# Optimization experiments

Hardware: AMD Instinct MI355X
Metric: run time of the kernel (lower is better)

## Reference

```python
import jax, jax.numpy as jnp
import numpy as np

N_CODES = 512
D = 8
BETA = 0.25


def setup_inputs() -> dict:
    key = jax.random.key(0)
    k1, k2 = jax.random.split(key)
    z = jax.random.normal(k1, (8, D, 16, 64, 64), dtype=jnp.float32)
    # torch init: uniform(-1/n_codes, 1/n_codes)
    codebook = jax.random.uniform(
        k2, (N_CODES, D), dtype=jnp.float32,
        minval=-1.0 / N_CODES, maxval=1.0 / N_CODES)
    return {"z": z, "codebook": codebook}


def reference(z, codebook):
    B, Dc, T, H, W = z.shape
    # [B, T, H, W, D] -> [N, D]
    z_flat = jnp.transpose(z, (0, 2, 3, 4, 1)).reshape(-1, Dc)
    z2 = jnp.sum(z_flat * z_flat, axis=1, keepdims=True)          # [N, 1]
    e2 = jnp.sum(codebook * codebook, axis=1)[None, :]            # [1, K]
    ze = z_flat @ codebook.T                                      # [N, K]
    dists = z2 + e2 - 2.0 * ze
    idx = jnp.argmin(dists, axis=1)                               # [N]
    z_q = jnp.transpose(codebook[idx].reshape(B, T, H, W, Dc), (0, 4, 1, 2, 3))
    commit = jnp.mean((jax.lax.stop_gradient(z_q) - z) ** 2)
    codebk = jnp.mean((z_q - jax.lax.stop_gradient(z)) ** 2)
    vq_loss = codebk + BETA * commit
    z_q_st = z + jax.lax.stop_gradient(z_q - z)
    return z_q_st, vq_loss, idx.reshape(B, T, H, W)
```

## Files before the change

kernel.cpp:

```cpp
#include <hip/hip_runtime.h>


#define NPTS      524288
#define KCODES    512
#define DDIM      8
#define CH_STRIDE 65536
#define B_STRIDE  524288
#define BLK       512
#define NWAVES    8
#define NTILES    32
#define CMAX      4
#define NLOSS     64
#define FLT_BIG   3.402823466e+38f

typedef short bf8 __attribute__((ext_vector_type(8)));
typedef float f4  __attribute__((ext_vector_type(4)));

__device__ __forceinline__ unsigned short f2bf(float f) {
    unsigned u = __float_as_uint(f);
    unsigned r = u + 0x7fffu + ((u >> 16) & 1u);
    return (unsigned short)(r >> 16);
}
__device__ __forceinline__ float bf2f(unsigned short h) {
    return __uint_as_float(((unsigned)h) << 16);
}

__device__ __forceinline__ float np_sumsq8(const float* x) {
    float p0 = __fmul_rn(x[0], x[0]);
    float p1 = __fmul_rn(x[1], x[1]);
    float p2 = __fmul_rn(x[2], x[2]);
    float p3 = __fmul_rn(x[3], x[3]);
    float p4 = __fmul_rn(x[4], x[4]);
    float p5 = __fmul_rn(x[5], x[5]);
    float p6 = __fmul_rn(x[6], x[6]);
    float p7 = __fmul_rn(x[7], x[7]);
    return __fadd_rn(__fadd_rn(__fadd_rn(p0, p1), __fadd_rn(p2, p3)),
                     __fadd_rn(__fadd_rn(p4, p5), __fadd_rn(p6, p7)));
}

__device__ __forceinline__ float np_dist(const float* __restrict__ cb,
                                         const float* __restrict__ e2f,
                                         int k, const float* zv, float z2) {
    const float* c = cb + (size_t)k * DDIM;
    float ze = 0.0f;
    #pragma unroll
    for (int j = 0; j < DDIM; ++j) ze = __fmaf_rn(zv[j], c[j], ze);
    return __fmaf_rn(-2.0f, ze, __fadd_rn(z2, e2f[k]));
}

__global__ void prep(const float* __restrict__ cb, float* __restrict__ e2f,
                     unsigned short* __restrict__ wsB,
                     float* __restrict__ loss_ws) {
    const int tid = blockIdx.x * 256 + threadIdx.x;
    if (tid < NLOSS) loss_ws[tid] = 0.0f;
    const int t    = tid >> 6;
    const int lane = tid & 63;
    const int quad = lane >> 4;
    const int colc = lane & 15;
    const int n    = t * 16 + colc;
    float row[DDIM];
    #pragma unroll
    for (int j = 0; j < DDIM; ++j) row[j] = cb[n * DDIM + j];
    const float e2 = np_sumsq8(row);
    if (quad == 3) e2f[n] = e2;

    unsigned short sh[8];
    #pragma unroll
    for (int j = 0; j < 8; ++j) {
        const unsigned short eh = f2bf(row[j]);
        const unsigned short el = f2bf(__fsub_rn(row[j], bf2f(eh)));
        sh[j] = (quad == 1) ? el : eh;
    }
    if (quad == 3) {
        const unsigned short e2h = f2bf(e2);
        const unsigned short e2l = f2bf(__fsub_rn(e2, bf2f(e2h)));
        sh[0] = e2h; sh[1] = e2l;
        #pragma unroll
        for (int j = 2; j < 8; ++j) sh[j] = 0;
    }
    unsigned short* dst = wsB + (size_t)(t * 64 + lane) * 8;
    #pragma unroll
    for (int j = 0; j < 8; ++j) dst[j] = sh[j];
}

__global__ __launch_bounds__(BLK, 4) void vq_main(
    const float* __restrict__ z, const float* __restrict__ cb,
    const float* __restrict__ e2f, const unsigned short* __restrict__ wsB,
    float* __restrict__ out_zq, float* __restrict__ loss_ws,
    float* __restrict__ out_idx)
{
    __shared__ int            ccnt[BLK];
    __shared__ unsigned short clist[BLK][CMAX];
    __shared__ float          wsum[NWAVES];

    const int tid  = threadIdx.x;
    const int wave = tid >> 6;
    const int lane = tid & 63;
    const int quad = lane >> 4;
    const int col  = lane & 15;

    ccnt[tid] = 0;

    const int n = blockIdx.x * BLK + tid;
    const int b = n >> 16;
    const int s = n & 65535;
    const float* zp = z + (size_t)b * B_STRIDE + s;
    float zv[DDIM];
    #pragma unroll
    for (int j = 0; j < DDIM; ++j) zv[j] = zp[(size_t)j * CH_STRIDE];
    const float z2 = np_sumsq8(zv);

    float zmax = z2;
    #pragma unroll
    for (int mk = 1; mk <= 32; mk <<= 1) zmax = fmaxf(zmax, __shfl_xor(zmax, mk, 64));
    const float eps = zmax * 6e-7f + 3e-6f;

    unsigned pkz[8];
    #pragma unroll
    for (int j = 0; j < 8; ++j) {
        const unsigned short hh = f2bf(zv[j]);
        const float zh = bf2f(hh);
        const float zl = __fsub_rn(zv[j], zh);
        const unsigned short ah = f2bf(-2.0f * zh);
        const unsigned short al = f2bf(-2.0f * zl);
        pkz[j] = (unsigned)ah | ((unsigned)al << 16);
    }

    bf8 af0, af1, af2, af3;
#define MK_AFRAG(AF, Q)                                                        \
    {                                                                          \
        const int srcl = (Q)*16 + col;                                         \
        _Pragma("unroll")                                                      \
        for (int j = 0; j < 8; ++j) {                                          \
            const unsigned w = (unsigned)__shfl((int)pkz[j], srcl, 64);        \
            const unsigned us = (quad == 2) ? (w >> 16) : (w & 0xFFFFu);       \
            AF[j] = (short)us;                                                 \
        }                                                                      \
        if (quad == 3) AF = (bf8){(short)0x3F80, (short)0x3F80, 0, 0, 0, 0, 0, 0}; \
    }
    MK_AFRAG(af0, 0) MK_AFRAG(af1, 1) MK_AFRAG(af2, 2) MK_AFRAG(af3, 3)

    const bf8* __restrict__ Bp = (const bf8*)wsB;

    f4 mn0 = (f4){FLT_BIG, FLT_BIG, FLT_BIG, FLT_BIG};
    f4 mn1 = mn0, mn2 = mn0, mn3 = mn0;
    #pragma unroll 4
    for (int t = 0; t < NTILES; ++t) {
        const bf8 bfrag = Bp[t * 64 + lane];
        f4 zero = (f4){0.0f, 0.0f, 0.0f, 0.0f};
        const f4 a0 = __builtin_amdgcn_mfma_f32_16x16x32_bf16(af0, bfrag, zero, 0, 0, 0);
        const f4 a1 = __builtin_amdgcn_mfma_f32_16x16x32_bf16(af1, bfrag, zero, 0, 0, 0);
        const f4 a2 = __builtin_amdgcn_mfma_f32_16x16x32_bf16(af2, bfrag, zero, 0, 0, 0);
        const f4 a3 = __builtin_amdgcn_mfma_f32_16x16x32_bf16(af3, bfrag, zero, 0, 0, 0);
        #pragma unroll
        for (int r = 0; r < 4; ++r) {
            mn0[r] = fminf(mn0[r], a0[r]); mn1[r] = fminf(mn1[r], a1[r]);
            mn2[r] = fminf(mn2[r], a2[r]); mn3[r] = fminf(mn3[r], a3[r]);
        }
    }
    #pragma unroll
    for (int mk = 1; mk <= 8; mk <<= 1) {
        #pragma unroll
        for (int r = 0; r < 4; ++r) {
            mn0[r] = fminf(mn0[r], __shfl_xor(mn0[r], mk, 64));
            mn1[r] = fminf(mn1[r], __shfl_xor(mn1[r], mk, 64));
            mn2[r] = fminf(mn2[r], __shfl_xor(mn2[r], mk, 64));
            mn3[r] = fminf(mn3[r], __shfl_xor(mn3[r], mk, 64));
        }
    }
    #pragma unroll
    for (int r = 0; r < 4; ++r) {
        mn0[r] += eps; mn1[r] += eps; mn2[r] += eps; mn3[r] += eps;
    }

    const int pbase = wave * 64 + quad * 4;
    #pragma unroll 4
    for (int t = 0; t < NTILES; ++t) {
        const bf8 bfrag = Bp[t * 64 + lane];
        f4 zero = (f4){0.0f, 0.0f, 0.0f, 0.0f};
        const f4 a0 = __builtin_amdgcn_mfma_f32_16x16x32_bf16(af0, bfrag, zero, 0, 0, 0);
        const f4 a1 = __builtin_amdgcn_mfma_f32_16x16x32_bf16(af1, bfrag, zero, 0, 0, 0);
        const f4 a2 = __builtin_amdgcn_mfma_f32_16x16x32_bf16(af2, bfrag, zero, 0, 0, 0);
        const f4 a3 = __builtin_amdgcn_mfma_f32_16x16x32_bf16(af3, bfrag, zero, 0, 0, 0);
        const unsigned short code = (unsigned short)(t * 16 + col);
#define PUSH(AQ, MQ, Q)                                                        \
    {                                                                          \
        const bool c0 = AQ[0] <= MQ[0], c1 = AQ[1] <= MQ[1];                   \
        const bool c2 = AQ[2] <= MQ[2], c3 = AQ[3] <= MQ[3];                   \
        if (c0 | c1 | c2 | c3) {                                               \
            const int pt = pbase + (Q)*16;                                     \
            if (c0) { int p = atomicAdd(&ccnt[pt + 0], 1); if (p < CMAX) clist[pt + 0][p] = code; } \
            if (c1) { int p = atomicAdd(&ccnt[pt + 1], 1); if (p < CMAX) clist[pt + 1][p] = code; } \
            if (c2) { int p = atomicAdd(&ccnt[pt + 2], 1); if (p < CMAX) clist[pt + 2][p] = code; } \
            if (c3) { int p = atomicAdd(&ccnt[pt + 3], 1); if (p < CMAX) clist[pt + 3][p] = code; } \
        }                                                                      \
    }
        PUSH(a0, mn0, 0) PUSH(a1, mn1, 1) PUSH(a2, mn2, 2) PUSH(a3, mn3, 3)
    }

    asm volatile("s_waitcnt lgkmcnt(0)" ::: "memory");

    const int cnt = ccnt[tid];
    int bidx;
    if (cnt == 1) {
        bidx = clist[tid][0];
    } else if (cnt <= CMAX) {
        float best = FLT_BIG; bidx = 0;
        for (int i = 0; i < cnt; ++i) {
            const int k = clist[tid][i];
            const float d = np_dist(cb, e2f, k, zv, z2);
            if (d < best || (d == best && k < bidx)) { best = d; bidx = k; }
        }
    } else {
        float best = FLT_BIG; bidx = 0;
        for (int k = 0; k < KCODES; ++k) {
            const float d = np_dist(cb, e2f, k, zv, z2);
            if (d < best) { best = d; bidx = k; }
        }
    }
    out_idx[n] = (float)bidx;

    const float* cw = cb + (size_t)bidx * DDIM;
    float* op = out_zq + (size_t)b * B_STRIDE + s;
    float lsum = 0.0f;
    #pragma unroll
    for (int j = 0; j < DDIM; ++j) {
        const float zq = cw[j];
        const float t  = __fsub_rn(zq, zv[j]);
        op[(size_t)j * CH_STRIDE] = __fadd_rn(zv[j], t);
        lsum = __fmaf_rn(t, t, lsum);
    }

    #pragma unroll
    for (int off = 32; off > 0; off >>= 1) lsum += __shfl_down(lsum, off, 64);
    if (lane == 0) wsum[wave] = lsum;
    __syncthreads();
    if (tid == 0) {
        float bs = 0.0f;
        #pragma unroll
        for (int w = 0; w < NWAVES; ++w) bs += wsum[w];
        atomicAdd(&loss_ws[blockIdx.x & (NLOSS - 1)], bs);
    }
}

__global__ void loss_fin(const float* __restrict__ loss_ws,
                         float* __restrict__ out_loss) {
    const int lane = threadIdx.x;
    float v = loss_ws[lane];
    #pragma unroll
    for (int off = 32; off > 0; off >>= 1) v += __shfl_down(v, off, 64);
    if (lane == 0) *out_loss = v * (1.25f / 4194304.0f);
}

extern "C" void kernel_launch(void* const* d_in, const int* in_sizes, int n_in,
                              void* d_out, int out_size, void* d_ws, size_t ws_size,
                              hipStream_t stream) {
    const float* z  = (const float*)d_in[0];
    const float* cb = (const float*)d_in[1];
    float* out      = (float*)d_out;
    float* out_zq   = out;
    float* out_loss = out + 4194304;
    float* out_idx  = out + 4194305;
    float* e2f            = (float*)d_ws;
    unsigned short* wsB   = (unsigned short*)((char*)d_ws + 2048);
    float* loss_ws        = (float*)((char*)d_ws + 2048 + 32768);

    prep<<<8, 256, 0, stream>>>(cb, e2f, wsB, loss_ws);
    vq_main<<<NPTS / BLK, BLK, 0, stream>>>(z, cb, e2f, wsB,
                                            out_zq, loss_ws, out_idx);
    loss_fin<<<1, 64, 0, stream>>>(loss_ws, out_loss);
}
```

Baseline: 123.7 us.

## Process two point sets per thread to reuse codebook fragments across MFMAs

Halves the block size to 256 threads while keeping 512 points per block, so each thread handles two points. Every codebook B-fragment loaded from global memory now feeds eight MFMAs instead of four, cutting fragment loads and loop overhead per point. The cost is roughly double the live registers (two sets of A fragments and running minima), which may lower occupancy. The launch bound changes to 256 threads with a minimum of 2 blocks.

```diff
diff --git a/kernel.cpp b/kernel.cpp
--- a/kernel.cpp
+++ b/kernel.cpp
@@ -6,8 +6,9 @@
 #define DDIM      8
 #define CH_STRIDE 65536
 #define B_STRIDE  524288
-#define BLK       512
-#define NWAVES    8
+#define BLK       256
+#define NWAVES    4
+#define PPB       512
 #define NTILES    32
 #define CMAX      4
 #define NLOSS     64
@@ -83,14 +84,14 @@
     for (int j = 0; j < 8; ++j) dst[j] = sh[j];
 }
 
-__global__ __launch_bounds__(BLK, 4) void vq_main(
+__global__ __launch_bounds__(BLK, 2) void vq_main(
     const float* __restrict__ z, const float* __restrict__ cb,
     const float* __restrict__ e2f, const unsigned short* __restrict__ wsB,
     float* __restrict__ out_zq, float* __restrict__ loss_ws,
     float* __restrict__ out_idx)
 {
-    __shared__ int            ccnt[BLK];
-    __shared__ unsigned short clist[BLK][CMAX];
+    __shared__ int            ccnt[PPB];
+    __shared__ unsigned short clist[PPB][CMAX];
     __shared__ float          wsum[NWAVES];
 
     const int tid  = threadIdx.x;
@@ -99,136 +100,197 @@
     const int quad = lane >> 4;
     const int col  = lane & 15;
 
-    ccnt[tid] = 0;
-
-    const int n = blockIdx.x * BLK + tid;
-    const int b = n >> 16;
-    const int s = n & 65535;
-    const float* zp = z + (size_t)b * B_STRIDE + s;
-    float zv[DDIM];
-    #pragma unroll
-    for (int j = 0; j < DDIM; ++j) zv[j] = zp[(size_t)j * CH_STRIDE];
-    const float z2 = np_sumsq8(zv);
-
-    float zmax = z2;
+    ccnt[tid]       = 0;
+    ccnt[tid + BLK] = 0;
+
+    const int base = blockIdx.x * PPB;
+    const int n0 = base + tid;
+    const int n1 = n0 + BLK;
+    const int b0 = n0 >> 16, s0 = n0 & 65535;
+    const int b1 = n1 >> 16, s1 = n1 & 65535;
+    const float* zp0 = z + (size_t)b0 * B_STRIDE + s0;
+    const float* zp1 = z + (size_t)b1 * B_STRIDE + s1;
+    float zva[DDIM], zvb[DDIM];
+    #pragma unroll
+    for (int j = 0; j < DDIM; ++j) {
+        zva[j] = zp0[(size_t)j * CH_STRIDE];
+        zvb[j] = zp1[(size_t)j * CH_STRIDE];
+    }
+    const float z2a = np_sumsq8(zva);
+    const float z2b = np_sumsq8(zvb);
+
+    float zmax = fmaxf(z2a, z2b);
     #pragma unroll
     for (int mk = 1; mk <= 32; mk <<= 1) zmax = fmaxf(zmax, __shfl_xor(zmax, mk, 64));
     const float eps = zmax * 6e-7f + 3e-6f;
 
-    unsigned pkz[8];
+    unsigned pka[8], pkb[8];
     #pragma unroll
     for (int j = 0; j < 8; ++j) {
-        const unsigned short hh = f2bf(zv[j]);
-        const float zh = bf2f(hh);
-        const float zl = __fsub_rn(zv[j], zh);
-        const unsigned short ah = f2bf(-2.0f * zh);
-        const unsigned short al = f2bf(-2.0f * zl);
-        pkz[j] = (unsigned)ah | ((unsigned)al << 16);
-    }
-
-    bf8 af0, af1, af2, af3;
-#define MK_AFRAG(AF, Q)                                                        \
+        {
+            const unsigned short hh = f2bf(zva[j]);
+            const float zh = bf2f(hh);
+            const float zl = __fsub_rn(zva[j], zh);
+            const unsigned short ah = f2bf(-2.0f * zh);
+            const unsigned short al = f2bf(-2.0f * zl);
+            pka[j] = (unsigned)ah | ((unsigned)al << 16);
+        }
+        {
+            const unsigned short hh = f2bf(zvb[j]);
+            const float zh = bf2f(hh);
+            const float zl = __fsub_rn(zvb[j], zh);
+            const unsigned short ah = f2bf(-2.0f * zh);
+            const unsigned short al = f2bf(-2.0f * zl);
+            pkb[j] = (unsigned)ah | ((unsigned)al << 16);
+        }
+    }
+
+    bf8 af0a, af1a, af2a, af3a, af0b, af1b, af2b, af3b;
+#define MK_AFRAG(AF, Q, PK)                                                    \
     {                                                                          \
         const int srcl = (Q)*16 + col;                                         \
         _Pragma("unroll")                                                      \
         for (int j = 0; j < 8; ++j) {                                          \
-            const unsigned w = (unsigned)__shfl((int)pkz[j], srcl, 64);        \
+            const unsigned w = (unsigned)__shfl((int)PK[j], srcl, 64);         \
             const unsigned us = (quad == 2) ? (w >> 16) : (w & 0xFFFFu);       \
             AF[j] = (short)us;                                                 \
         }                                                                      \
         if (quad == 3) AF = (bf8){(short)0x3F80, (short)0x3F80, 0, 0, 0, 0, 0, 0}; \
     }
-    MK_AFRAG(af0, 0) MK_AFRAG(af1, 1) MK_AFRAG(af2, 2) MK_AFRAG(af3, 3)
+    MK_AFRAG(af0a, 0, pka) MK_AFRAG(af1a, 1, pka)
+    MK_AFRAG(af2a, 2, pka) MK_AFRAG(af3a, 3, pka)
+    MK_AFRAG(af0b, 0, pkb) MK_AFRAG(af1b, 1, pkb)
+    MK_AFRAG(af2b, 2, pkb) MK_AFRAG(af3b, 3, pkb)
 
     const bf8* __restrict__ Bp = (const bf8*)wsB;
 
-    f4 mn0 = (f4){FLT_BIG, FLT_BIG, FLT_BIG, FLT_BIG};
-    f4 mn1 = mn0, mn2 = mn0, mn3 = mn0;
-    #pragma unroll 4
+    f4 mA0 = (f4){FLT_BIG, FLT_BIG, FLT_BIG, FLT_BIG};
+    f4 mA1 = mA0, mA2 = mA0, mA3 = mA0;
+    f4 mB0 = mA0, mB1 = mA0, mB2 = mA0, mB3 = mA0;
+    #pragma unroll 2
     for (int t = 0; t < NTILES; ++t) {
         const bf8 bfrag = Bp[t * 64 + lane];
         f4 zero = (f4){0.0f, 0.0f, 0.0f, 0.0f};
-        const f4 a0 = __builtin_amdgcn_mfma_f32_16x16x32_bf16(af0, bfrag, zero, 0, 0, 0);
-        const f4 a1 = __builtin_amdgcn_mfma_f32_16x16x32_bf16(af1, bfrag, zero, 0, 0, 0);
-        const f4 a2 = __builtin_amdgcn_mfma_f32_16x16x32_bf16(af2, bfrag, zero, 0, 0, 0);
-        const f4 a3 = __builtin_amdgcn_mfma_f32_16x16x32_bf16(af3, bfrag, zero, 0, 0, 0);
+        const f4 dA0 = __builtin_amdgcn_mfma_f32_16x16x32_bf16(af0a, bfrag, zero, 0, 0, 0);
+        const f4 dA1 = __builtin_amdgcn_mfma_f32_16x16x32_bf16(af1a, bfrag, zero, 0, 0, 0);
+        const f4 dA2 = __builtin_amdgcn_mfma_f32_16x16x32_bf16(af2a, bfrag, zero, 0, 0, 0);
+        const f4 dA3 = __builtin_amdgcn_mfma_f32_16x16x32_bf16(af3a, bfrag, zero, 0, 0, 0);
+        const f4 dB0 = __builtin_amdgcn_mfma_f32_16x16x32_bf16(af0b, bfrag, zero, 0, 0, 0);
+        const f4 dB1 = __builtin_amdgcn_mfma_f32_16x16x32_bf16(af1b, bfrag, zero, 0, 0, 0);
+        const f4 dB2 = __builtin_amdgcn_mfma_f32_16x16x32_bf16(af2b, bfrag, zero, 0, 0, 0);
+        const f4 dB3 = __builtin_amdgcn_mfma_f32_16x16x32_bf16(af3b, bfrag, zero, 0, 0, 0);
         #pragma unroll
         for (int r = 0; r < 4; ++r) {
-            mn0[r] = fminf(mn0[r], a0[r]); mn1[r] = fminf(mn1[r], a1[r]);
-            mn2[r] = fminf(mn2[r], a2[r]); mn3[r] = fminf(mn3[r], a3[r]);
+            mA0[r] = fminf(mA0[r], dA0[r]); mA1[r] = fminf(mA1[r], dA1[r]);
+            mA2[r] = fminf(mA2[r], dA2[r]); mA3[r] = fminf(mA3[r], dA3[r]);
+            mB0[r] = fminf(mB0[r], dB0[r]); mB1[r] = fminf(mB1[r], dB1[r]);
+            mB2[r] = fminf(mB2[r], dB2[r]); mB3[r] = fminf(mB3[r], dB3[r]);
         }
     }
     #pragma unroll
     for (int mk = 1; mk <= 8; mk <<= 1) {
         #pragma unroll
         for (int r = 0; r < 4; ++r) {
-            mn0[r] = fminf(mn0[r], __shfl_xor(mn0[r], mk, 64));
-            mn1[r] = fminf(mn1[r], __shfl_xor(mn1[r], mk, 64));
-            mn2[r] = fminf(mn2[r], __shfl_xor(mn2[r], mk, 64));
-            mn3[r] = fminf(mn3[r], __shfl_xor(mn3[r], mk, 64));
+            mA0[r] = fminf(mA0[r], __shfl_xor(mA0[r], mk, 64));
+            mA1[r] = fminf(mA1[r], __shfl_xor(mA1[r], mk, 64));
+            mA2[r] = fminf(mA2[r], __shfl_xor(mA2[r], mk, 64));
+            mA3[r] = fminf(mA3[r], __shfl_xor(mA3[r], mk, 64));
+            mB0[r] = fminf(mB0[r], __shfl_xor(mB0[r], mk, 64));
+            mB1[r] = fminf(mB1[r], __shfl_xor(mB1[r], mk, 64));
+            mB2[r] = fminf(mB2[r], __shfl_xor(mB2[r], mk, 64));
+            mB3[r] = fminf(mB3[r], __shfl_xor(mB3[r], mk, 64));
         }
     }
     #pragma unroll
     for (int r = 0; r < 4; ++r) {
-        mn0[r] += eps; mn1[r] += eps; mn2[r] += eps; mn3[r] += eps;
-    }
-
-    const int pbase = wave * 64 + quad * 4;
-    #pragma unroll 4
+        mA0[r] += eps; mA1[r] += eps; mA2[r] += eps; mA3[r] += eps;
+        mB0[r] += eps; mB1[r] += eps; mB2[r] += eps; mB3[r] += eps;
+    }
+
+    const int pb0 = wave * 64 + quad * 4;
+    const int pb1 = BLK + pb0;
+    #pragma unroll 2
     for (int t = 0; t < NTILES; ++t) {
         const bf8 bfrag = Bp[t * 64 + lane];
         f4 zero = (f4){0.0f, 0.0f, 0.0f, 0.0f};
-        const f4 a0 = __builtin_amdgcn_mfma_f32_16x16x32_bf16(af0, bfrag, zero, 0, 0, 0);
-        const f4 a1 = __builtin_amdgcn_mfma_f32_16x16x32_bf16(af1, bfrag, zero, 0, 0, 0);
-        const f4 a2 = __builtin_amdgcn_mfma_f32_16x16x32_bf16(af2, bfrag, zero, 0, 0, 0);
-        const f4 a3 = __builtin_amdgcn_mfma_f32_16x16x32_bf16(af3, bfrag, zero, 0, 0, 0);
+        const f4 dA0 = __builtin_amdgcn_mfma_f32_16x16x32_bf16(af0a, bfrag, zero, 0, 0, 0);
+        const f4 dA1 = __builtin_amdgcn_mfma_f32_16x16x32_bf16(af1a, bfrag, zero, 0, 0, 0);
+        const f4 dA2 = __builtin_amdgcn_mfma_f32_16x16x32_bf16(af2a, bfrag, zero, 0, 0, 0);
+        const f4 dA3 = __builtin_amdgcn_mfma_f32_16x16x32_bf16(af3a, bfrag, zero, 0, 0, 0);
+        const f4 dB0 = __builtin_amdgcn_mfma_f32_16x16x32_bf16(af0b, bfrag, zero, 0, 0, 0);
+        const f4 dB1 = __builtin_amdgcn_mfma_f32_16x16x32_bf16(af1b, bfrag, zero, 0, 0, 0);
+        const f4 dB2 = __builtin_amdgcn_mfma_f32_16x16x32_bf16(af2b, bfrag, zero, 0, 0, 0);
+        const f4 dB3 = __builtin_amdgcn_mfma_f32_16x16x32_bf16(af3b, bfrag, zero, 0, 0, 0);
         const unsigned short code = (unsigned short)(t * 16 + col);
-#define PUSH(AQ, MQ, Q)                                                        \
+#define PUSH(AQ, MQ, Q, PB)                                                    \
     {                                                                          \
         const bool c0 = AQ[0] <= MQ[0], c1 = AQ[1] <= MQ[1];                   \
         const bool c2 = AQ[2] <= MQ[2], c3 = AQ[3] <= MQ[3];                   \
         if (c0 | c1 | c2 | c3) {                                               \
-            const int pt = pbase + (Q)*16;                                     \
+            const int pt = (PB) + (Q)*16;                                      \
             if (c0) { int p = atomicAdd(&ccnt[pt + 0], 1); if (p < CMAX) clist[pt + 0][p] = code; } \
             if (c1) { int p = atomicAdd(&ccnt[pt + 1], 1); if (p < CMAX) clist[pt + 1][p] = code; } \
             if (c2) { int p = atomicAdd(&ccnt[pt + 2], 1); if (p < CMAX) clist[pt + 2][p] = code; } \
             if (c3) { int p = atomicAdd(&ccnt[pt + 3], 1); if (p < CMAX) clist[pt + 3][p] = code; } \
         }                                                                      \
     }
-        PUSH(a0, mn0, 0) PUSH(a1, mn1, 1) PUSH(a2, mn2, 2) PUSH(a3, mn3, 3)
+        PUSH(dA0, mA0, 0, pb0) PUSH(dA1, mA1, 1, pb0)
+        PUSH(dA2, mA2, 2, pb0) PUSH(dA3, mA3, 3, pb0)
+        PUSH(dB0, mB0, 0, pb1) PUSH(dB1, mB1, 1, pb1)
+        PUSH(dB2, mB2, 2, pb1) PUSH(dB3, mB3, 3, pb1)
     }
 
     asm volatile("s_waitcnt lgkmcnt(0)" ::: "memory");
 
-    const int cnt = ccnt[tid];
-    int bidx;
-    if (cnt == 1) {
-        bidx = clist[tid][0];
-    } else if (cnt <= CMAX) {
-        float best = FLT_BIG; bidx = 0;
-        for (int i = 0; i < cnt; ++i) {
-            const int k = clist[tid][i];
-            const float d = np_dist(cb, e2f, k, zv, z2);
-            if (d < best || (d == best && k < bidx)) { best = d; bidx = k; }
-        }
-    } else {
-        float best = FLT_BIG; bidx = 0;
-        for (int k = 0; k < KCODES; ++k) {
-            const float d = np_dist(cb, e2f, k, zv, z2);
-            if (d < best) { best = d; bidx = k; }
-        }
-    }
-    out_idx[n] = (float)bidx;
-
-    const float* cw = cb + (size_t)bidx * DDIM;
-    float* op = out_zq + (size_t)b * B_STRIDE + s;
+    auto resolve = [&](int slot, const float* zv, float z2) -> int {
+        const int cnt = ccnt[slot];
+        int bidx;
+        if (cnt == 1) {
+            bidx = clist[slot][0];
+        } else if (cnt <= CMAX) {
+            float best = FLT_BIG; bidx = 0;
+            for (int i = 0; i < cnt; ++i) {
+                const int k = clist[slot][i];
+                const float d = np_dist(cb, e2f, k, zv, z2);
+                if (d < best || (d == best && k < bidx)) { best = d; bidx = k; }
+            }
+        } else {
+            float best = FLT_BIG; bidx = 0;
+            for (int k = 0; k < KCODES; ++k) {
+                const float d = np_dist(cb, e2f, k, zv, z2);
+                if (d < best) { best = d; bidx = k; }
+            }
+        }
+        return bidx;
+    };
+
+    const int bidx0 = resolve(tid, zva, z2a);
+    const int bidx1 = resolve(tid + BLK, zvb, z2b);
+    out_idx[n0] = (float)bidx0;
+    out_idx[n1] = (float)bidx1;
+
     float lsum = 0.0f;
-    #pragma unroll
-    for (int j = 0; j < DDIM; ++j) {
-        const float zq = cw[j];
-        const float t  = __fsub_rn(zq, zv[j]);
-        op[(size_t)j * CH_STRIDE] = __fadd_rn(zv[j], t);
-        lsum = __fmaf_rn(t, t, lsum);
+    {
+        const float* cw = cb + (size_t)bidx0 * DDIM;
+        float* op = out_zq + (size_t)b0 * B_STRIDE + s0;
+        #pragma unroll
+        for (int j = 0; j < DDIM; ++j) {
+            const float zq = cw[j];
+            const float t  = __fsub_rn(zq, zva[j]);
+            op[(size_t)j * CH_STRIDE] = __fadd_rn(zva[j], t);
+            lsum = __fmaf_rn(t, t, lsum);
+        }
+    }
+    {
+        const float* cw = cb + (size_t)bidx1 * DDIM;
+        float* op = out_zq + (size_t)b1 * B_STRIDE + s1;
+        #pragma unroll
+        for (int j = 0; j < DDIM; ++j) {
+            const float zq = cw[j];
+            const float t  = __fsub_rn(zq, zvb[j]);
+            op[(size_t)j * CH_STRIDE] = __fadd_rn(zvb[j], t);
+            lsum = __fmaf_rn(t, t, lsum);
+        }
     }
 
     #pragma unroll
@@ -266,7 +328,7 @@
     float* loss_ws        = (float*)((char*)d_ws + 2048 + 32768);
 
     prep<<<8, 256, 0, stream>>>(cb, e2f, wsB, loss_ws);
-    vq_main<<<NPTS / BLK, BLK, 0, stream>>>(z, cb, e2f, wsB,
+    vq_main<<<NPTS / PPB, BLK, 0, stream>>>(z, cb, e2f, wsB,
                                             out_zq, loss_ws, out_idx);
     loss_fin<<<1, 64, 0, stream>>>(loss_ws, out_loss);
 }
```

Measured after the change: 148.1 us. +19.7%, slower.

## Stage codebook B-fragments in LDS and double-buffer two tiles per iteration

Applied to the files above, without the earlier changes.

Copies the pre-packed bf16 codebook fragments (32 KB) from global memory into shared memory once per block, then reads B fragments from LDS instead of global/L2. Both MFMA passes now process two tiles per iteration with register prefetch of the next pair and a combined min-check before candidate pushes. CMAX is raised to 8 so fewer points fall back to the full 512-code scan. The extra 32 KB of LDS per block plus the larger candidate list may reduce occupancy below the launch-bounds target of 4 blocks.

```diff
diff --git a/kernel.cpp b/kernel.cpp
--- a/kernel.cpp
+++ b/kernel.cpp
@@ -9,7 +9,7 @@
 #define BLK       512
 #define NWAVES    8
 #define NTILES    32
-#define CMAX      4
+#define CMAX      8
 #define NLOSS     64
 #define FLT_BIG   3.402823466e+38f
 
@@ -89,6 +89,7 @@
     float* __restrict__ out_zq, float* __restrict__ loss_ws,
     float* __restrict__ out_idx)
 {
+    __shared__ unsigned short ldsB[NTILES * 64 * 8];
     __shared__ int            ccnt[BLK];
     __shared__ unsigned short clist[BLK][CMAX];
     __shared__ float          wsum[NWAVES];
@@ -99,8 +100,6 @@
     const int quad = lane >> 4;
     const int col  = lane & 15;
 
-    ccnt[tid] = 0;
-
     const int n = blockIdx.x * BLK + tid;
     const int b = n >> 16;
     const int s = n & 65535;
@@ -108,6 +107,16 @@
     float zv[DDIM];
     #pragma unroll
     for (int j = 0; j < DDIM; ++j) zv[j] = zp[(size_t)j * CH_STRIDE];
+
+    {
+        const uint4* src = (const uint4*)wsB;
+        uint4* dst = (uint4*)ldsB;
+        #pragma unroll
+        for (int q = 0; q < 4; ++q)
+            dst[tid + q * BLK] = src[tid + q * BLK];
+    }
+    ccnt[tid] = 0;
+
     const float z2 = np_sumsq8(zv);
 
     float zmax = z2;
@@ -140,22 +149,30 @@
     }
     MK_AFRAG(af0, 0) MK_AFRAG(af1, 1) MK_AFRAG(af2, 2) MK_AFRAG(af3, 3)
 
-    const bf8* __restrict__ Bp = (const bf8*)wsB;
+    __syncthreads();
+
+    const bf8* __restrict__ Bp = (const bf8*)ldsB;
+    const f4 zero = (f4){0.0f, 0.0f, 0.0f, 0.0f};
 
     f4 mn0 = (f4){FLT_BIG, FLT_BIG, FLT_BIG, FLT_BIG};
     f4 mn1 = mn0, mn2 = mn0, mn3 = mn0;
-    #pragma unroll 4
-    for (int t = 0; t < NTILES; ++t) {
-        const bf8 bfrag = Bp[t * 64 + lane];
-        f4 zero = (f4){0.0f, 0.0f, 0.0f, 0.0f};
-        const f4 a0 = __builtin_amdgcn_mfma_f32_16x16x32_bf16(af0, bfrag, zero, 0, 0, 0);
-        const f4 a1 = __builtin_amdgcn_mfma_f32_16x16x32_bf16(af1, bfrag, zero, 0, 0, 0);
-        const f4 a2 = __builtin_amdgcn_mfma_f32_16x16x32_bf16(af2, bfrag, zero, 0, 0, 0);
-        const f4 a3 = __builtin_amdgcn_mfma_f32_16x16x32_bf16(af3, bfrag, zero, 0, 0, 0);
-        #pragma unroll
-        for (int r = 0; r < 4; ++r) {
-            mn0[r] = fminf(mn0[r], a0[r]); mn1[r] = fminf(mn1[r], a1[r]);
-            mn2[r] = fminf(mn2[r], a2[r]); mn3[r] = fminf(mn3[r], a3[r]);
+    {
+        bf8 bA = Bp[lane];
+        bf8 bB = Bp[64 + lane];
+        #pragma unroll 1
+        for (int t = 0; t < NTILES; t += 2) {
+            const bf8 cA = bA, cB = bB;
+            bA = Bp[(((t + 2) & 31) * 64) + lane];
+            bB = Bp[(((t + 3) & 31) * 64) + lane];
+            f4 dA, dB;
+#define P1Q(AF, MN)                                                            \
+            dA = __builtin_amdgcn_mfma_f32_16x16x32_bf16(AF, cA, zero, 0, 0, 0); \
+            dB = __builtin_amdgcn_mfma_f32_16x16x32_bf16(AF, cB, zero, 0, 0, 0); \
+            _Pragma("unroll")                                                  \
+            for (int r = 0; r < 4; ++r)                                        \
+                MN[r] = fminf(fminf(MN[r], dA[r]), dB[r]);
+            P1Q(af0, mn0) P1Q(af1, mn1) P1Q(af2, mn2) P1Q(af3, mn3)
+#undef P1Q
         }
     }
     #pragma unroll
@@ -174,28 +191,42 @@
     }
 
     const int pbase = wave * 64 + quad * 4;
-    #pragma unroll 4
-    for (int t = 0; t < NTILES; ++t) {
-        const bf8 bfrag = Bp[t * 64 + lane];
-        f4 zero = (f4){0.0f, 0.0f, 0.0f, 0.0f};
-        const f4 a0 = __builtin_amdgcn_mfma_f32_16x16x32_bf16(af0, bfrag, zero, 0, 0, 0);
-        const f4 a1 = __builtin_amdgcn_mfma_f32_16x16x32_bf16(af1, bfrag, zero, 0, 0, 0);
-        const f4 a2 = __builtin_amdgcn_mfma_f32_16x16x32_bf16(af2, bfrag, zero, 0, 0, 0);
-        const f4 a3 = __builtin_amdgcn_mfma_f32_16x16x32_bf16(af3, bfrag, zero, 0, 0, 0);
-        const unsigned short code = (unsigned short)(t * 16 + col);
-#define PUSH(AQ, MQ, Q)                                                        \
-    {                                                                          \
-        const bool c0 = AQ[0] <= MQ[0], c1 = AQ[1] <= MQ[1];                   \
-        const bool c2 = AQ[2] <= MQ[2], c3 = AQ[3] <= MQ[3];                   \
-        if (c0 | c1 | c2 | c3) {                                               \
-            const int pt = pbase + (Q)*16;                                     \
-            if (c0) { int p = atomicAdd(&ccnt[pt + 0], 1); if (p < CMAX) clist[pt + 0][p] = code; } \
-            if (c1) { int p = atomicAdd(&ccnt[pt + 1], 1); if (p < CMAX) clist[pt + 1][p] = code; } \
-            if (c2) { int p = atomicAdd(&ccnt[pt + 2], 1); if (p < CMAX) clist[pt + 2][p] = code; } \
-            if (c3) { int p = atomicAdd(&ccnt[pt + 3], 1); if (p < CMAX) clist[pt + 3][p] = code; } \
-        }                                                                      \
-    }
-        PUSH(a0, mn0, 0) PUSH(a1, mn1, 1) PUSH(a2, mn2, 2) PUSH(a3, mn3, 3)
+#define PUSHC(SLOT, CODE)                                                      \
+    { int p = atomicAdd(&ccnt[SLOT], 1); if (p < CMAX) clist[SLOT][p] = (unsigned short)(CODE); }
+    {
+        bf8 bA = Bp[lane];
+        bf8 bB = Bp[64 + lane];
+        #pragma unroll 1
+        for (int t = 0; t < NTILES; t += 2) {
+            const bf8 cA = bA, cB = bB;
+            bA = Bp[(((t + 2) & 31) * 64) + lane];
+            bB = Bp[(((t + 3) & 31) * 64) + lane];
+            const int codeA = t * 16 + col;
+            const int codeB = codeA + 16;
+            f4 dA, dB;
+#define P2Q(AF, MN, Q)                                                         \
+            dA = __builtin_amdgcn_mfma_f32_16x16x32_bf16(AF, cA, zero, 0, 0, 0); \
+            dB = __builtin_amdgcn_mfma_f32_16x16x32_bf16(AF, cB, zero, 0, 0, 0); \
+            {                                                                  \
+                const bool h0 = fminf(dA[0], dB[0]) <= MN[0];                  \
+                const bool h1 = fminf(dA[1], dB[1]) <= MN[1];                  \
+                const bool h2 = fminf(dA[2], dB[2]) <= MN[2];                  \
+                const bool h3 = fminf(dA[3], dB[3]) <= MN[3];                  \
+                if (h0 | h1 | h2 | h3) {                                       \
+                    const int pt = pbase + (Q)*16;                             \
+                    if (h0) { if (dA[0] <= MN[0]) PUSHC(pt + 0, codeA)         \
+                              if (dB[0] <= MN[0]) PUSHC(pt + 0, codeB) }       \
+                    if (h1) { if (dA[1] <= MN[1]) PUSHC(pt + 1, codeA)         \
+                              if (dB[1] <= MN[1]) PUSHC(pt + 1, codeB) }       \
+                    if (h2) { if (dA[2] <= MN[2]) PUSHC(pt + 2, codeA)         \
+                              if (dB[2] <= MN[2]) PUSHC(pt + 2, codeB) }       \
+                    if (h3) { if (dA[3] <= MN[3]) PUSHC(pt + 3, codeA)         \
+                              if (dB[3] <= MN[3]) PUSHC(pt + 3, codeB) }       \
+                }                                                              \
+            }
+            P2Q(af0, mn0, 0) P2Q(af1, mn1, 1) P2Q(af2, mn2, 2) P2Q(af3, mn3, 3)
+#undef P2Q
+        }
     }
 
     asm volatile("s_waitcnt lgkmcnt(0)" ::: "memory");
```

Result: slower. 127.8 us (+3.3%).
